# Kernel tuning notes

Measured on AMD Instinct MI355X. Metric: run time of the kernel, lower is better.

## Reference

```python
import jax, jax.numpy as jnp
import numpy as np

N_A, N_B, E, D = 200_000, 50_000, 1_000_000, 128


def setup_inputs() -> dict:
    key = jax.random.key(0)
    ks = jax.random.split(key, 10)
    s = 0.05  # weight scale
    return {
        "row_embs_a": jax.random.normal(ks[0], (N_A, D), jnp.float32),
        "row_embs_b": jax.random.normal(ks[1], (N_B, D), jnp.float32),
        "W_fwd": jax.random.normal(ks[2], (D, D), jnp.float32) * s,  # relation A:fk->B
        "b_fwd": jax.random.normal(ks[3], (D,), jnp.float32) * s,
        "W_rev": jax.random.normal(ks[4], (D, D), jnp.float32) * s,  # relation B:fk->A
        "b_rev": jax.random.normal(ks[5], (D,), jnp.float32) * s,
        "W_gate": jax.random.normal(ks[6], (D, 2 * D), jnp.float32) * s,  # shared_gate: Linear(2D, D)
        "b_gate": jax.random.normal(ks[7], (D,), jnp.float32) * s,
        "src_idx": jax.random.randint(ks[8], (E,), 0, N_A, jnp.int32),
        "dst_idx": jax.random.randint(ks[9], (E,), 0, N_B, jnp.int32),
    }


def reference(row_embs_a, row_embs_b, W_fwd, b_fwd, W_rev, b_rev, W_gate, b_gate, src_idx, dst_idx):
    """Faithful vectorized version of MultiTableImputer.propagate_observed_fk for two
    tables A, B connected by relation A:fk->B (with reverse B:fk->A registered)."""
    n_a = row_embs_a.shape[0]
    n_b = row_embs_b.shape[0]
    ones = jnp.ones(src_idx.shape, row_embs_a.dtype)

    # forward messages A -> B: gather, per-relation linear, scatter-add
    msg_fwd = row_embs_a[src_idx] @ W_fwd.T + b_fwd            # [E, D]
    agg_b = jax.ops.segment_sum(msg_fwd, dst_idx, num_segments=n_b)
    cnt_b = jax.ops.segment_sum(ones, dst_idx, num_segments=n_b)

    # reverse messages B -> A
    msg_rev = row_embs_b[dst_idx] @ W_rev.T + b_rev            # [E, D]
    agg_a = jax.ops.segment_sum(msg_rev, src_idx, num_segments=n_a)
    cnt_a = jax.ops.segment_sum(ones, src_idx, num_segments=n_a)

    def fuse(row, agg, cnt):
        mean_msg = agg / jnp.maximum(cnt, 1.0)[:, None]        # clamp(min=1)
        gate = jax.nn.sigmoid(jnp.concatenate([row, mean_msg], axis=-1) @ W_gate.T + b_gate)
        return gate * row + (1.0 - gate) * mean_msg

    return fuse(row_embs_a, agg_a, cnt_a), fuse(row_embs_b, agg_b, cnt_b)
```

## Files before the change

kernel.cpp:

```cpp
#include <hip/hip_runtime.h>
#include <math.h>

#define DD 128

typedef __attribute__((ext_vector_type(8))) short short8;
typedef __attribute__((ext_vector_type(4))) float f32x4;
typedef __attribute__((ext_vector_type(4))) unsigned short us4;
typedef __attribute__((ext_vector_type(8))) unsigned short us8;

__device__ __forceinline__ unsigned short f2bf(float f) {
  unsigned int u = __builtin_bit_cast(unsigned int, f);
  u = (u + 0x7FFFu + ((u >> 16) & 1u)) >> 16;
  return (unsigned short)u;
}

__device__ __forceinline__ float b2f(unsigned short u) {
  return __builtin_bit_cast(float, ((unsigned)u) << 16);
}

__global__ __launch_bounds__(256) void rowconv_kernel(
    const float* __restrict__ A, const float* __restrict__ B,
    unsigned short* __restrict__ dst, int nA4, int ntot4)
{
  int stride = gridDim.x * 256;
  for (int i = blockIdx.x * 256 + threadIdx.x; i < ntot4; i += stride) {
    float4 v = (i < nA4) ? ((const float4*)A)[i] : ((const float4*)B)[i - nA4];
    us4 o;
    o[0] = f2bf(v.x); o[1] = f2bf(v.y); o[2] = f2bf(v.z); o[3] = f2bf(v.w);
    ((us4*)dst)[i] = o;
  }
}

__global__ __launch_bounds__(256) void wconv_kernel(
    const float* __restrict__ Wrev, const float* __restrict__ Wfwd,
    const float* __restrict__ Wgate, unsigned short* __restrict__ dst)
{
  int i = blockIdx.x * 256 + threadIdx.x;
  float v;
  if (i < 16384) v = Wrev[i];
  else if (i < 32768) v = Wfwd[i - 16384];
  else {
    int j = (i - 32768) >> 7, k = (i - 32768) & 127;
    v = Wgate[j * 256 + k];
  }
  dst[i] = f2bf(v);
}

__global__ __launch_bounds__(128) void wc_kernel(
    const float* __restrict__ Wgate, const float* __restrict__ Wr,
    const float* __restrict__ br, unsigned short* __restrict__ Wc_bf,
    float* __restrict__ v)
{
  int j = blockIdx.x, k = threadIdx.x;
  const float* g2 = Wgate + (size_t)j * 256 + 128;
  float acc = 0.f;
  for (int m = 0; m < 128; ++m) acc += g2[m] * Wr[m * 128 + k];
  Wc_bf[j * 128 + k] = f2bf(acc);
  if (k == 0) {
    float a = 0.f;
    for (int m = 0; m < 128; ++m) a += g2[m] * br[m];
    v[j] = a;
  }
}

__global__ __launch_bounds__(256) void binhist_kernel(
    const int* __restrict__ src, const int* __restrict__ dst,
    int* __restrict__ binraw, int na_bins, int nbins, int E)
{
  __shared__ int h[1024];
  int t = threadIdx.x;
  for (int i = t; i < 1024; i += 256) h[i] = 0;
  __syncthreads();
  int stride = gridDim.x * 256;
  for (int e = blockIdx.x * 256 + t; e < E; e += stride) {
    int s = src[e], d = dst[e];
    atomicAdd(&h[s >> 10], 1);
    atomicAdd(&h[na_bins + (d >> 8)], 1);
  }
  __syncthreads();
  for (int i = t; i < nbins; i += 256)
    if (h[i]) atomicAdd(&binraw[i], h[i]);
}

__global__ __launch_bounds__(512) void binscan_kernel(
    const int* __restrict__ binraw, int nbins,
    int* __restrict__ binstart, int* __restrict__ bincur)
{
  __shared__ int buf[512];
  int t = threadIdx.x;
  int v = (t < nbins) ? binraw[t] : 0;
  buf[t] = v;
  __syncthreads();
  for (int off = 1; off < 512; off <<= 1) {
    int x = (t >= off) ? buf[t - off] : 0;
    __syncthreads();
    buf[t] += x;
    __syncthreads();
  }
  if (t < nbins) {
    int excl = buf[t] - v;
    binstart[t] = excl;
    bincur[t] = excl;
  }
}

__global__ __launch_bounds__(512) void binfill_kernel(
    const int* __restrict__ src, const int* __restrict__ dst,
    int* __restrict__ bincur, uint2* __restrict__ binrec,
    int n_a, int na_bins, int nbins, int E)
{
  __shared__ int lcnt[1024];
  __shared__ int goff[1024];
  const int t = threadIdx.x;
  const int base = blockIdx.x * 4096;
  for (int i = t; i < 1024; i += 512) lcnt[i] = 0;
  __syncthreads();

  int bins[16], ranks[16];
  unsigned keys[16], vals[16];
  #pragma unroll
  for (int j = 0; j < 8; ++j) {
    int e = base + j * 512 + t;
    int i0 = 2 * j, i1 = 2 * j + 1;
    if (e < E) {
      int s = src[e], d = dst[e];
      bins[i0] = s >> 10;               keys[i0] = (unsigned)s;       vals[i0] = (unsigned)d;
      bins[i1] = na_bins + (d >> 8);    keys[i1] = (unsigned)(n_a + d); vals[i1] = (unsigned)s;
      ranks[i0] = atomicAdd(&lcnt[bins[i0]], 1);
      ranks[i1] = atomicAdd(&lcnt[bins[i1]], 1);
    } else {
      bins[i0] = -1; bins[i1] = -1;
      ranks[i0] = 0;  ranks[i1] = 0;
      keys[i0] = 0;   keys[i1] = 0;
      vals[i0] = 0;   vals[i1] = 0;
    }
  }
  __syncthreads();
  for (int b = t; b < nbins; b += 512)
    if (lcnt[b]) goff[b] = atomicAdd(&bincur[b], lcnt[b]);
  __syncthreads();
  #pragma unroll
  for (int i = 0; i < 16; ++i) {
    if (bins[i] >= 0) {
      int p = goff[bins[i]] + ranks[i];
      binrec[p] = make_uint2(keys[i], vals[i]);
    }
  }
}

__global__ __launch_bounds__(256) void binscatter2_kernel(
    const uint2* __restrict__ binrec, const int* __restrict__ binstart,
    const int* __restrict__ binend, int* __restrict__ partner,
    int* __restrict__ start, int* __restrict__ cnt,
    int n_a, int n_total, int na_bins)
{
  __shared__ int cntL[1024];
  __shared__ int curL[1024];
  __shared__ int sbuf[256];
  const int b = blockIdx.x;
  const int t = threadIdx.x;
  int row0, nrows;
  if (b < na_bins) { row0 = b << 10; nrows = min(1024, n_a - row0); }
  else { row0 = n_a + ((b - na_bins) << 8); nrows = min(256, n_total - row0); }
  const int s0 = binstart[b], e0 = binend[b];

  for (int i = t; i < 1024; i += 256) cntL[i] = 0;
  __syncthreads();
  for (int i = s0 + t; i < e0; i += 256)
    atomicAdd(&cntL[binrec[i].x - (unsigned)row0], 1);
  __syncthreads();
  int l0 = cntL[4 * t], l1 = cntL[4 * t + 1];
  int l2 = cntL[4 * t + 2], l3 = cntL[4 * t + 3];
  int s = l0 + l1 + l2 + l3;
  sbuf[t] = s;
  __syncthreads();
  for (int off = 1; off < 256; off <<= 1) {
    int x = (t >= off) ? sbuf[t - off] : 0;
    __syncthreads();
    sbuf[t] += x;
    __syncthreads();
  }
  int excl = sbuf[t] - s;
  curL[4 * t]     = excl;
  curL[4 * t + 1] = excl + l0;
  curL[4 * t + 2] = excl + l0 + l1;
  curL[4 * t + 3] = excl + l0 + l1 + l2;
  __syncthreads();
  for (int j = t; j < nrows; j += 256) {
    start[row0 + j] = s0 + curL[j];
    cnt[row0 + j] = cntL[j];
  }
  __syncthreads();
  for (int i = s0 + t; i < e0; i += 256) {
    uint2 r = binrec[i];
    int pos = atomicAdd(&curL[r.x - (unsigned)row0], 1);
    partner[s0 + pos] = (int)r.y;
  }
}

__global__ __launch_bounds__(256) void aggregate_mean_bf16_kernel(
    const unsigned short* __restrict__ A_bf,
    const unsigned short* __restrict__ B_bf,
    const int* __restrict__ partner, const int* __restrict__ start,
    const int* __restrict__ cnt, unsigned short* __restrict__ mean_bf,
    int n_a, int n_total)
{
  int wid = (blockIdx.x * 256 + threadIdx.x) >> 6;
  if (wid >= n_total) return;
  int lane = threadIdx.x & 63;
  int q    = lane & 15;
  int quad = lane >> 4;
  int s0 = start[wid], c = cnt[wid];
  const unsigned short* tbl = (wid < n_a) ? B_bf : A_bf;
  float a0 = 0.f, a1 = 0.f, a2 = 0.f, a3 = 0.f;
  float a4 = 0.f, a5 = 0.f, a6 = 0.f, a7 = 0.f;
  int k = 0;
  for (; k + 16 <= c; k += 16) {
    int p0 = partner[s0 + k + 0 + quad];
    int p1 = partner[s0 + k + 4 + quad];
    int p2 = partner[s0 + k + 8 + quad];
    int p3 = partner[s0 + k + 12 + quad];
    us8 v0 = *(const us8*)(tbl + (size_t)p0 * DD + 8 * q);
    us8 v1 = *(const us8*)(tbl + (size_t)p1 * DD + 8 * q);
    us8 v2 = *(const us8*)(tbl + (size_t)p2 * DD + 8 * q);
    us8 v3 = *(const us8*)(tbl + (size_t)p3 * DD + 8 * q);
    a0 += b2f(v0[0]) + b2f(v1[0]) + b2f(v2[0]) + b2f(v3[0]);
    a1 += b2f(v0[1]) + b2f(v1[1]) + b2f(v2[1]) + b2f(v3[1]);
    a2 += b2f(v0[2]) + b2f(v1[2]) + b2f(v2[2]) + b2f(v3[2]);
    a3 += b2f(v0[3]) + b2f(v1[3]) + b2f(v2[3]) + b2f(v3[3]);
    a4 += b2f(v0[4]) + b2f(v1[4]) + b2f(v2[4]) + b2f(v3[4]);
    a5 += b2f(v0[5]) + b2f(v1[5]) + b2f(v2[5]) + b2f(v3[5]);
    a6 += b2f(v0[6]) + b2f(v1[6]) + b2f(v2[6]) + b2f(v3[6]);
    a7 += b2f(v0[7]) + b2f(v1[7]) + b2f(v2[7]) + b2f(v3[7]);
  }
  for (; k < c; k += 4) {
    int i = k + quad;
    if (i < c) {
      int p = partner[s0 + i];
      us8 v = *(const us8*)(tbl + (size_t)p * DD + 8 * q);
      a0 += b2f(v[0]); a1 += b2f(v[1]); a2 += b2f(v[2]); a3 += b2f(v[3]);
      a4 += b2f(v[4]); a5 += b2f(v[5]); a6 += b2f(v[6]); a7 += b2f(v[7]);
    }
  }
  a0 += __shfl_xor(a0, 16); a0 += __shfl_xor(a0, 32);
  a1 += __shfl_xor(a1, 16); a1 += __shfl_xor(a1, 32);
  a2 += __shfl_xor(a2, 16); a2 += __shfl_xor(a2, 32);
  a3 += __shfl_xor(a3, 16); a3 += __shfl_xor(a3, 32);
  a4 += __shfl_xor(a4, 16); a4 += __shfl_xor(a4, 32);
  a5 += __shfl_xor(a5, 16); a5 += __shfl_xor(a5, 32);
  a6 += __shfl_xor(a6, 16); a6 += __shfl_xor(a6, 32);
  a7 += __shfl_xor(a7, 16); a7 += __shfl_xor(a7, 32);
  if (lane < 16) {
    float inv = (c > 0) ? (1.f / (float)c) : 0.f;
    us8 o;
    o[0] = f2bf(a0 * inv); o[1] = f2bf(a1 * inv);
    o[2] = f2bf(a2 * inv); o[3] = f2bf(a3 * inv);
    o[4] = f2bf(a4 * inv); o[5] = f2bf(a5 * inv);
    o[6] = f2bf(a6 * inv); o[7] = f2bf(a7 * inv);
    *(us8*)&mean_bf[(size_t)wid * DD + 8 * q] = o;
  }
}

__global__ __launch_bounds__(512) void fused_post_kernel(
    const unsigned short* __restrict__ rows16,
    const unsigned short* __restrict__ mean_bf,
    const int* __restrict__ cnt,
    const unsigned short* __restrict__ Wr_bf,
    const unsigned short* __restrict__ Wg1_bf,
    const unsigned short* __restrict__ Wc_bf,
    const float* __restrict__ br, const float* __restrict__ bg,
    const float* __restrict__ vv,
    float* __restrict__ out, int n)
{
  __shared__ unsigned short Wr_l[128 * 128];
  __shared__ unsigned short Wg1_l[128 * 128];
  __shared__ unsigned short Wc_l[128 * 128];
  __shared__ float br_l[128];
  __shared__ float bg_l[128];
  __shared__ float v_l[128];

  const int t = threadIdx.x;
  for (int oi = t; oi < 2048; oi += 512) {
    int j = oi >> 4, o = oi & 15;
    int d = j * 128 + ((o ^ (j & 15)) << 3);
    *(short8*)&Wr_l[d]  = *(const short8*)&Wr_bf[oi << 3];
    *(short8*)&Wg1_l[d] = *(const short8*)&Wg1_bf[oi << 3];
    *(short8*)&Wc_l[d]  = *(const short8*)&Wc_bf[oi << 3];
  }
  if (t < 128) { br_l[t] = br[t]; bg_l[t] = bg[t]; v_l[t] = vv[t]; }
  __syncthreads();

  const int wid  = t >> 6;
  const int lane = t & 63;
  const int lrow = lane & 15;
  const int lgrp = lane >> 4;
  const int m0 = blockIdx.x * 128 + wid * 16;
  if (m0 >= n) return;

  const int mr = m0 + lrow;
  const bool rowok = mr < n;

  short8 am[4], ar[4];
  #pragma unroll
  for (int ks = 0; ks < 4; ++ks) {
    short8 z = {0, 0, 0, 0, 0, 0, 0, 0};
    am[ks] = z; ar[ks] = z;
    if (rowok) {
      size_t off = (size_t)mr * DD + ks * 32 + lgrp * 8;
      am[ks] = *(const short8*)&mean_bf[off];
      ar[ks] = *(const short8*)&rows16[off];
    }
  }

  f32x4 tac[8];
  #pragma unroll
  for (int jt = 0; jt < 8; ++jt) {
    float bv = br_l[jt * 16 + lrow];
    f32x4 c = {bv, bv, bv, bv};
    #pragma unroll
    for (int ks = 0; ks < 4; ++ks) {
      int o = ks * 4 + lgrp;
      short8 b = *(short8*)&Wr_l[(jt * 16 + lrow) * 128 + ((o ^ lrow) << 3)];
      c = __builtin_amdgcn_mfma_f32_16x16x32_bf16(am[ks], b, c, 0, 0, 0);
    }
    tac[jt] = c;
  }

  const int rbase = m0 + lgrp * 4;
  int cv4[4];
  #pragma unroll
  for (int r = 0; r < 4; ++r) {
    int rr = rbase + r;
    cv4[r] = (rr < n) ? cnt[rr] : 0;
    if (cv4[r] == 0) {
      #pragma unroll
      for (int jt = 0; jt < 8; ++jt) tac[jt][r] = 0.f;
    }
  }

  #pragma unroll
  for (int jt = 0; jt < 8; ++jt) {
    int col = jt * 16 + lrow;
    float bgc = bg_l[col];
    float bgv = bgc + v_l[col];
    f32x4 c;
    #pragma unroll
    for (int r = 0; r < 4; ++r) c[r] = (cv4[r] > 0) ? bgv : bgc;
    #pragma unroll
    for (int ks = 0; ks < 4; ++ks) {
      int o = ks * 4 + lgrp;
      short8 b = *(short8*)&Wg1_l[(jt * 16 + lrow) * 128 + ((o ^ lrow) << 3)];
      c = __builtin_amdgcn_mfma_f32_16x16x32_bf16(ar[ks], b, c, 0, 0, 0);
    }
    #pragma unroll
    for (int ks = 0; ks < 4; ++ks) {
      int o = ks * 4 + lgrp;
      short8 b = *(short8*)&Wc_l[(jt * 16 + lrow) * 128 + ((o ^ lrow) << 3)];
      c = __builtin_amdgcn_mfma_f32_16x16x32_bf16(am[ks], b, c, 0, 0, 0);
    }
    #pragma unroll
    for (int r = 0; r < 4; ++r) {
      int rr = rbase + r;
      if (rr < n) {
        float g = 1.f / (1.f + __expf(-c[r]));
        float rowf = b2f(rows16[(size_t)rr * DD + col]);
        out[(size_t)rr * DD + col] = g * rowf + (1.f - g) * tac[jt][r];
      }
    }
  }
}

extern "C" void kernel_launch(void* const* d_in, const int* in_sizes, int n_in,
                              void* d_out, int out_size, void* d_ws, size_t ws_size,
                              hipStream_t stream) {
  const float* A      = (const float*)d_in[0];
  const float* B      = (const float*)d_in[1];
  const float* W_fwd  = (const float*)d_in[2];
  const float* b_fwd  = (const float*)d_in[3];
  const float* W_rev  = (const float*)d_in[4];
  const float* b_rev  = (const float*)d_in[5];
  const float* W_gate = (const float*)d_in[6];
  const float* b_gate = (const float*)d_in[7];
  const int*   src    = (const int*)d_in[8];
  const int*   dst    = (const int*)d_in[9];

  const int n_a = in_sizes[0] / DD;
  const int n_b = in_sizes[1] / DD;
  const int E   = in_sizes[8];
  const int n_total = n_a + n_b;

  const int na_bins = (n_a + 1023) >> 10;
  const int nb_bins = (n_b + 255) >> 8;
  const int nbins   = na_bins + nb_bins;

  float* out = (float*)d_out;

  int* cnt      = (int*)d_ws;
  int* binraw   = cnt + n_total;
  int* start    = binraw + 1024;
  int* binstart = start + n_total;
  int* bincur   = binstart + 1024;
  uint2* binrec = (uint2*)(bincur + 1024);
  int* partner  = (int*)(binrec + 2 * (size_t)E);
  uintptr_t wp = (uintptr_t)(partner + 2 * (size_t)E);
  wp = (wp + 63) & ~(uintptr_t)63;
  unsigned short* wbf = (unsigned short*)wp;
  float* vab = (float*)(wbf + 81920);
  unsigned short* rows_bf = (unsigned short*)(vab + 256);
  unsigned short* A_bf = rows_bf;
  unsigned short* B_bf = rows_bf + (size_t)n_a * DD;
  unsigned short* mean_bf = rows_bf + (size_t)n_total * DD;

  const int nA4  = n_a * (DD / 4);
  const int nt4  = n_total * (DD / 4);

  hipMemsetAsync(binraw, 0, 1024 * sizeof(int), stream);

  rowconv_kernel<<<2048, 256, 0, stream>>>(A, B, rows_bf, nA4, nt4);
  wconv_kernel<<<192, 256, 0, stream>>>(W_rev, W_fwd, W_gate, wbf);
  wc_kernel<<<128, 128, 0, stream>>>(W_gate, W_rev, b_rev, wbf + 49152, vab);
  wc_kernel<<<128, 128, 0, stream>>>(W_gate, W_fwd, b_fwd, wbf + 65536, vab + 128);

  binhist_kernel<<<1024, 256, 0, stream>>>(src, dst, binraw, na_bins, nbins, E);
  binscan_kernel<<<1, 512, 0, stream>>>(binraw, nbins, binstart, bincur);
  binfill_kernel<<<(E + 4095) / 4096, 512, 0, stream>>>(
      src, dst, bincur, binrec, n_a, na_bins, nbins, E);
  binscatter2_kernel<<<nbins, 256, 0, stream>>>(
      binrec, binstart, bincur, partner, start, cnt, n_a, n_total, na_bins);

  aggregate_mean_bf16_kernel<<<(n_total + 3) / 4, 256, 0, stream>>>(
      A_bf, B_bf, partner, start, cnt, mean_bf, n_a, n_total);

  fused_post_kernel<<<(n_a + 127) / 128, 512, 0, stream>>>(
      A_bf, mean_bf, cnt, wbf, wbf + 32768, wbf + 49152,
      b_rev, b_gate, vab, out, n_a);
  fused_post_kernel<<<(n_b + 127) / 128, 512, 0, stream>>>(
      B_bf, mean_bf + (size_t)n_a * DD, cnt + n_a, wbf + 16384, wbf + 32768,
      wbf + 65536, b_fwd, b_gate, vab + 128,
      out + (size_t)n_a * DD, n_b);
}
```

Baseline: 334.1 us.

## Merge A/B post kernels into one launch and drop Wc shared-memory staging

The two fused_post launches (table A and table B) become a single grid, with each block choosing its table's pointers from its block index. This removes one launch and the tail gap between them. The Wc weight matrix is no longer staged in LDS and is read from global memory inside the MFMA loop instead. That cuts LDS per block from about 96KB to about 64KB, and launch_bounds(512,4) is added to raise occupancy. The cost is more global/L2 traffic for the Wc operand.

```diff
diff --git a/kernel.cpp b/kernel.cpp
--- a/kernel.cpp
+++ b/kernel.cpp
@@ -261,40 +261,50 @@
   }
 }
 
-__global__ __launch_bounds__(512) void fused_post_kernel(
-    const unsigned short* __restrict__ rows16,
+__global__ __launch_bounds__(512, 4) void fused_post_kernel(
+    const unsigned short* __restrict__ rows_bf,
     const unsigned short* __restrict__ mean_bf,
     const int* __restrict__ cnt,
-    const unsigned short* __restrict__ Wr_bf,
-    const unsigned short* __restrict__ Wg1_bf,
-    const unsigned short* __restrict__ Wc_bf,
-    const float* __restrict__ br, const float* __restrict__ bg,
-    const float* __restrict__ vv,
-    float* __restrict__ out, int n)
+    const unsigned short* __restrict__ wbf,
+    const float* __restrict__ b_rev, const float* __restrict__ b_fwd,
+    const float* __restrict__ bg, const float* __restrict__ vab,
+    float* __restrict__ out, int n_a, int n_b, int gA)
 {
   __shared__ unsigned short Wr_l[128 * 128];
   __shared__ unsigned short Wg1_l[128 * 128];
-  __shared__ unsigned short Wc_l[128 * 128];
   __shared__ float br_l[128];
   __shared__ float bg_l[128];
   __shared__ float v_l[128];
 
   const int t = threadIdx.x;
+  const bool isB = (int)blockIdx.x >= gA;
+  const int bid = isB ? ((int)blockIdx.x - gA) : (int)blockIdx.x;
+  const int n   = isB ? n_b : n_a;
+  const size_t roff = isB ? (size_t)n_a * DD : 0;
+  const unsigned short* rowsp = rows_bf + roff;
+  const unsigned short* meanp = mean_bf + roff;
+  const int* cntp = cnt + (isB ? n_a : 0);
+  float* outp = out + roff;
+  const unsigned short* Wr_g  = wbf + (isB ? 16384 : 0);
+  const unsigned short* Wg1_g = wbf + 32768;
+  const unsigned short* Wc_g  = wbf + 49152 + (isB ? 16384 : 0);
+  const float* brp = isB ? b_fwd : b_rev;
+  const float* vp  = vab + (isB ? 128 : 0);
+
   for (int oi = t; oi < 2048; oi += 512) {
     int j = oi >> 4, o = oi & 15;
     int d = j * 128 + ((o ^ (j & 15)) << 3);
-    *(short8*)&Wr_l[d]  = *(const short8*)&Wr_bf[oi << 3];
-    *(short8*)&Wg1_l[d] = *(const short8*)&Wg1_bf[oi << 3];
-    *(short8*)&Wc_l[d]  = *(const short8*)&Wc_bf[oi << 3];
-  }
-  if (t < 128) { br_l[t] = br[t]; bg_l[t] = bg[t]; v_l[t] = vv[t]; }
+    *(short8*)&Wr_l[d]  = *(const short8*)&Wr_g[oi << 3];
+    *(short8*)&Wg1_l[d] = *(const short8*)&Wg1_g[oi << 3];
+  }
+  if (t < 128) { br_l[t] = brp[t]; bg_l[t] = bg[t]; v_l[t] = vp[t]; }
   __syncthreads();
 
   const int wid  = t >> 6;
   const int lane = t & 63;
   const int lrow = lane & 15;
   const int lgrp = lane >> 4;
-  const int m0 = blockIdx.x * 128 + wid * 16;
+  const int m0 = bid * 128 + wid * 16;
   if (m0 >= n) return;
 
   const int mr = m0 + lrow;
@@ -307,8 +317,8 @@
     am[ks] = z; ar[ks] = z;
     if (rowok) {
       size_t off = (size_t)mr * DD + ks * 32 + lgrp * 8;
-      am[ks] = *(const short8*)&mean_bf[off];
-      ar[ks] = *(const short8*)&rows16[off];
+      am[ks] = *(const short8*)&meanp[off];
+      ar[ks] = *(const short8*)&rowsp[off];
     }
   }
 
@@ -331,7 +341,7 @@
   #pragma unroll
   for (int r = 0; r < 4; ++r) {
     int rr = rbase + r;
-    cv4[r] = (rr < n) ? cnt[rr] : 0;
+    cv4[r] = (rr < n) ? cntp[rr] : 0;
     if (cv4[r] == 0) {
       #pragma unroll
       for (int jt = 0; jt < 8; ++jt) tac[jt][r] = 0.f;
@@ -354,8 +364,8 @@
     }
     #pragma unroll
     for (int ks = 0; ks < 4; ++ks) {
-      int o = ks * 4 + lgrp;
-      short8 b = *(short8*)&Wc_l[(jt * 16 + lrow) * 128 + ((o ^ lrow) << 3)];
+      short8 b = *(const short8*)&Wc_g[(size_t)(jt * 16 + lrow) * 128 +
+                                       (ks * 4 + lgrp) * 8];
       c = __builtin_amdgcn_mfma_f32_16x16x32_bf16(am[ks], b, c, 0, 0, 0);
     }
     #pragma unroll
@@ -363,8 +373,8 @@
       int rr = rbase + r;
       if (rr < n) {
         float g = 1.f / (1.f + __expf(-c[r]));
-        float rowf = b2f(rows16[(size_t)rr * DD + col]);
-        out[(size_t)rr * DD + col] = g * rowf + (1.f - g) * tac[jt][r];
+        float rowf = b2f(rowsp[(size_t)rr * DD + col]);
+        outp[(size_t)rr * DD + col] = g * rowf + (1.f - g) * tac[jt][r];
       }
     }
   }
@@ -431,11 +441,9 @@
   aggregate_mean_bf16_kernel<<<(n_total + 3) / 4, 256, 0, stream>>>(
       A_bf, B_bf, partner, start, cnt, mean_bf, n_a, n_total);
 
-  fused_post_kernel<<<(n_a + 127) / 128, 512, 0, stream>>>(
-      A_bf, mean_bf, cnt, wbf, wbf + 32768, wbf + 49152,
-      b_rev, b_gate, vab, out, n_a);
-  fused_post_kernel<<<(n_b + 127) / 128, 512, 0, stream>>>(
-      B_bf, mean_bf + (size_t)n_a * DD, cnt + n_a, wbf + 16384, wbf + 32768,
-      wbf + 65536, b_fwd, b_gate, vab + 128,
-      out + (size_t)n_a * DD, n_b);
-}
+  const int gA = (n_a + 127) / 128;
+  const int gB = (n_b + 127) / 128;
+  fused_post_kernel<<<gA + gB, 512, 0, stream>>>(
+      rows_bf, mean_bf, cnt, wbf, b_rev, b_fwd, b_gate, vab,
+      out, n_a, n_b, gA);
+}
```

New measurement: 332.2 us. No clear change (-0.6%).
